# Kernel tuning notes

Measured on AMD Instinct MI355X. Metric: run time of the kernel, lower is better.

Reference implementation:

```python
import jax, jax.numpy as jnp
import numpy as np

GRAVITY, MAIN_THRUST, SIDE_TORQUE, DT = 10.0, 6.0, 1.0, 0.02
H_OBS = jnp.array([[1, 0, 0, 0, 0, 0],
                   [0, 1, 0, 0, 0, 0],
                   [0, 0, 0, 0, 1, 0]], dtype=jnp.float32)  # (3,6)


def build_psd(log_diag, off_diag, dim):
    rows, cols = np.tril_indices(dim, -1)  # row-major, same order as torch.tril_indices
    L = jnp.zeros((dim, dim), dtype=log_diag.dtype)
    L = L.at[jnp.arange(dim), jnp.arange(dim)].set(jnp.exp(log_diag))
    L = L.at[rows, cols].set(off_diag)
    return L @ L.T + 1e-6 * jnp.eye(dim, dtype=log_diag.dtype)


def setup_inputs() -> dict:
    key = jax.random.key(0)
    B = 524288
    ks = jax.random.split(key, 8)
    z = jax.random.normal(ks[0], (B, 3), dtype=jnp.float32)
    u = jax.random.uniform(ks[1], (B, 2), dtype=jnp.float32)
    x_prev = jax.random.normal(ks[2], (B, 6), dtype=jnp.float32)
    A = 0.1 * jax.random.normal(ks[3], (B, 6, 6), dtype=jnp.float32)
    P_prev = jnp.einsum('bij,bkj->bik', A, A) + 0.5 * jnp.eye(6, dtype=jnp.float32)
    q_log_diag = jnp.array([-3.0, -3.0, -2.0, -2.0, -3.0, -2.0], dtype=jnp.float32)
    q_off_diag = 0.01 * jax.random.normal(ks[4], (15,), dtype=jnp.float32)
    r_log_diag = jnp.array([-2.0, -2.0, -2.0], dtype=jnp.float32)
    r_off_diag = 0.01 * jax.random.normal(ks[5], (3,), dtype=jnp.float32)
    return {"z": z, "u": u, "x_prev": x_prev, "P_prev": P_prev,
            "q_log_diag": q_log_diag, "q_off_diag": q_off_diag,
            "r_log_diag": r_log_diag, "r_off_diag": r_off_diag}


def _dynamics(x, u):
    px, py, vx, vy, theta, omega = (x[:, i] for i in range(6))
    main_power = jnp.clip(u[:, 0], 0.0, 1.0)
    lateral = u[:, 1]
    sin_th, cos_th = jnp.sin(theta), jnp.cos(theta)
    ax = -MAIN_THRUST * sin_th * main_power
    ay = MAIN_THRUST * cos_th * main_power - GRAVITY
    alpha = SIDE_TORQUE * lateral
    new_vx = vx + ax * DT
    new_vy = vy + ay * DT
    new_omega = omega + alpha * DT
    new_px = px + new_vx * DT
    new_py = py + new_vy * DT
    new_theta = theta + new_omega * DT
    return jnp.stack([new_px, new_py, new_vx, new_vy, new_theta, new_omega], axis=-1)


def _dynamics_jacobian(x, u):
    B = x.shape[0]
    theta = x[:, 4]
    main_power = jnp.clip(u[:, 0], 0.0, 1.0)
    sin_th, cos_th = jnp.sin(theta), jnp.cos(theta)
    Tm = MAIN_THRUST * main_power
    d = jnp.arange(6)
    F = jnp.zeros((B, 6, 6), dtype=x.dtype).at[:, d, d].set(1.0)
    F = F.at[:, 0, 2].set(DT).at[:, 1, 3].set(DT).at[:, 4, 5].set(DT)
    F = F.at[:, 2, 4].set(-Tm * cos_th * DT)
    F = F.at[:, 3, 4].set(-Tm * sin_th * DT)
    F = F.at[:, 0, 4].set(-Tm * cos_th * (DT * DT))
    F = F.at[:, 1, 4].set(-Tm * sin_th * (DT * DT))
    return F


def reference(z, u, x_prev, P_prev, q_log_diag, q_off_diag, r_log_diag, r_off_diag):
    Q = build_psd(q_log_diag, q_off_diag, 6)
    R = build_psd(r_log_diag, r_off_diag, 3)
    H = H_OBS
    # predict
    x_pred = _dynamics(x_prev, u)                              # (B,6)
    F = _dynamics_jacobian(x_prev, u)                          # (B,6,6)
    P_pred = jnp.einsum('bij,bjk,blk->bil', F, P_prev, F) + Q  # F P F^T + Q
    # update
    z_pred = jnp.einsum('ij,bj->bi', H, x_pred)                # (B,3)
    y = z - z_pred
    HP = jnp.einsum('ij,bjk->bik', H, P_pred)                  # (B,3,6)
    S = jnp.einsum('bij,kj->bik', HP, H) + R                   # (B,3,3)
    K = jnp.swapaxes(jnp.linalg.solve(S, HP), -1, -2)          # (B,6,3)
    x_upd = x_pred + jnp.einsum('bij,bj->bi', K, y)
    IKH = jnp.eye(6, dtype=x_pred.dtype) - jnp.einsum('bij,jk->bik', K, H)
    P_upd = (jnp.einsum('bij,bjk,blk->bil', IKH, P_pred, IKH)
             + jnp.einsum('bij,jk,blk->bil', K, R, K))          # Joseph form
    return (x_upd, P_upd)
```

## Files before the change

### kernel.cpp

```cpp
#include <hip/hip_runtime.h>

namespace {
constexpr float GRAVITY     = 10.0f;
constexpr float MAIN_THRUST = 6.0f;
constexpr float DT          = 0.02f;
constexpr int   BLK         = 128;
constexpr int   ROWPAD      = 44;
}

__global__ void qr_precompute(const float* __restrict__ qld,
                              const float* __restrict__ qod,
                              const float* __restrict__ rld,
                              const float* __restrict__ rod,
                              float* __restrict__ out)
{
    if (threadIdx.x != 0 || blockIdx.x != 0) return;
    float L[6][6];
    for (int i = 0; i < 6; ++i)
        for (int j = 0; j < 6; ++j) L[i][j] = 0.0f;
    for (int i = 0; i < 6; ++i) L[i][i] = expf(qld[i]);
    L[1][0] = qod[0];
    L[2][0] = qod[1];  L[2][1] = qod[2];
    L[3][0] = qod[3];  L[3][1] = qod[4];  L[3][2] = qod[5];
    L[4][0] = qod[6];  L[4][1] = qod[7];  L[4][2] = qod[8];  L[4][3] = qod[9];
    L[5][0] = qod[10]; L[5][1] = qod[11]; L[5][2] = qod[12]; L[5][3] = qod[13];
    L[5][4] = qod[14];
    for (int i = 0; i < 6; ++i)
        for (int j = 0; j < 6; ++j) {
            float s = 0.0f;
            const int m = i < j ? i : j;
            for (int k = 0; k <= m; ++k) s += L[i][k] * L[j][k];
            if (i == j) s += 1e-6f;
            out[i * 6 + j] = s;
        }
    const float rd0 = expf(rld[0]), rd1 = expf(rld[1]), rd2 = expf(rld[2]);
    const float ro0 = rod[0], ro1 = rod[1], ro2 = rod[2];
    out[36] = rd0 * rd0 + 1e-6f;
    out[37] = ro0 * rd0;
    out[38] = ro0 * ro0 + rd1 * rd1 + 1e-6f;
    out[39] = ro1 * rd0;
    out[40] = ro1 * ro0 + ro2 * rd1;
    out[41] = ro1 * ro1 + ro2 * ro2 + rd2 * rd2 + 1e-6f;
}

__global__ __launch_bounds__(BLK) void ekf_kernel(
    const float* __restrict__ z,
    const float* __restrict__ u,
    const float* __restrict__ x_prev,
    const float* __restrict__ P_prev,
    const float* __restrict__ qr,
    float* __restrict__ x_out,
    float* __restrict__ P_out,
    int B)
{
    __shared__ float smem[BLK * ROWPAD];

    const int t = threadIdx.x;
    const long long blockElem0 = (long long)blockIdx.x * BLK;
    const long long elemsLeft  = (long long)B - blockElem0;
    const int nElem  = elemsLeft >= BLK ? BLK : (int)elemsLeft;
    const int count4 = nElem * 9;

    {
        const float4* gP4 = reinterpret_cast<const float4*>(P_prev + blockElem0 * 36);
        #pragma unroll
        for (int k = 0; k < 9; ++k) {
            const int g4 = t + k * BLK;
            if (g4 < count4) {
                const float4 v = gP4[g4];
                const int elem = g4 / 9;
                const int off4 = g4 % 9;
                *reinterpret_cast<float4*>(&smem[elem * ROWPAD + off4 * 4]) = v;
            }
        }
    }
    __syncthreads();

    const bool valid = (t < nElem);
    const long long b = blockElem0 + t;

    if (valid) {
        const float R00 = qr[36], R10 = qr[37], R11 = qr[38];
        const float R20 = qr[39], R21 = qr[40], R22 = qr[41];

        const float2* xp2 = reinterpret_cast<const float2*>(x_prev + 6 * b);
        const float2 x01 = xp2[0], x23 = xp2[1], x45 = xp2[2];
        const float px = x01.x, py = x01.y, vx = x23.x, vy = x23.y;
        const float th = x45.x, om = x45.y;

        const float2 uu = *reinterpret_cast<const float2*>(u + 2 * b);
        const float mp  = fminf(fmaxf(uu.x, 0.0f), 1.0f);
        const float lat = uu.y;

        float s_th, c_th;
        __sincosf(th, &s_th, &c_th);

        const float Tm  = MAIN_THRUST * mp;
        const float ax  = -Tm * s_th;
        const float ay  =  Tm * c_th - GRAVITY;
        const float nvx = vx + ax * DT;
        const float nvy = vy + ay * DT;
        const float nom = om + lat * DT;
        const float npx = px + nvx * DT;
        const float npy = py + nvy * DT;
        const float nth = th + nom * DT;
        const float xp[6] = {npx, npy, nvx, nvy, nth, nom};

        const float f24 = -Tm * c_th * DT;
        const float f34 = -Tm * s_th * DT;
        const float f04 = f24 * DT;
        const float f14 = f34 * DT;

        float P[36];
        const float* myrow = &smem[t * ROWPAD];
        #pragma unroll
        for (int k = 0; k < 9; ++k) {
            const float4 v = *reinterpret_cast<const float4*>(&myrow[k * 4]);
            P[4 * k + 0] = v.x; P[4 * k + 1] = v.y;
            P[4 * k + 2] = v.z; P[4 * k + 3] = v.w;
        }

        #pragma unroll
        for (int j = 0; j < 6; ++j) {
            P[0 * 6 + j] += DT * P[2 * 6 + j] + f04 * P[4 * 6 + j];
            P[1 * 6 + j] += DT * P[3 * 6 + j] + f14 * P[4 * 6 + j];
            P[2 * 6 + j] += f24 * P[4 * 6 + j];
            P[3 * 6 + j] += f34 * P[4 * 6 + j];
            P[4 * 6 + j] += DT * P[5 * 6 + j];
        }
        #pragma unroll
        for (int i = 0; i < 6; ++i) {
            const float m0 = P[i * 6 + 0], m1 = P[i * 6 + 1], m2 = P[i * 6 + 2];
            const float m3 = P[i * 6 + 3], m4 = P[i * 6 + 4], m5 = P[i * 6 + 5];
            P[i * 6 + 0] = m0 + DT * m2 + f04 * m4 + qr[i * 6 + 0];
            P[i * 6 + 1] = m1 + DT * m3 + f14 * m4 + qr[i * 6 + 1];
            P[i * 6 + 2] = m2 + f24 * m4 + qr[i * 6 + 2];
            P[i * 6 + 3] = m3 + f34 * m4 + qr[i * 6 + 3];
            P[i * 6 + 4] = m4 + DT * m5 + qr[i * 6 + 4];
            P[i * 6 + 5] = m5 + qr[i * 6 + 5];
        }

        const float* zp = z + 3 * b;
        const float y0 = zp[0] - npx;
        const float y1 = zp[1] - npy;
        const float y2 = zp[2] - nth;

        const float s00 = P[0 * 6 + 0] + R00;
        const float s01 = P[0 * 6 + 1] + R10;
        const float s02 = P[0 * 6 + 4] + R20;
        const float s10 = P[1 * 6 + 0] + R10;
        const float s11 = P[1 * 6 + 1] + R11;
        const float s12 = P[1 * 6 + 4] + R21;
        const float s20 = P[4 * 6 + 0] + R20;
        const float s21 = P[4 * 6 + 1] + R21;
        const float s22 = P[4 * 6 + 4] + R22;

        const float det = s00 * (s11 * s22 - s12 * s21)
                        + s01 * (s12 * s20 - s10 * s22)
                        + s02 * (s10 * s21 - s11 * s20);
        const float invd = 1.0f / det;
        const float i00 = (s11 * s22 - s12 * s21) * invd;
        const float i01 = (s02 * s21 - s01 * s22) * invd;
        const float i02 = (s01 * s12 - s02 * s11) * invd;
        const float i10 = (s12 * s20 - s10 * s22) * invd;
        const float i11 = (s00 * s22 - s02 * s20) * invd;
        const float i12 = (s02 * s10 - s00 * s12) * invd;
        const float i20 = (s10 * s21 - s11 * s20) * invd;
        const float i21 = (s01 * s20 - s00 * s21) * invd;
        const float i22 = (s00 * s11 - s01 * s10) * invd;

        float r0[6], r1[6], r4[6];
        #pragma unroll
        for (int j = 0; j < 6; ++j) {
            r0[j] = P[0 * 6 + j];
            r1[j] = P[1 * 6 + j];
            r4[j] = P[4 * 6 + j];
        }

        float K[6][3];
        #pragma unroll
        for (int i = 0; i < 6; ++i) {
            const float hp0 = r0[i], hp1 = r1[i], hp2 = r4[i];
            K[i][0] = i00 * hp0 + i01 * hp1 + i02 * hp2;
            K[i][1] = i10 * hp0 + i11 * hp1 + i12 * hp2;
            K[i][2] = i20 * hp0 + i21 * hp1 + i22 * hp2;
        }

        float2* xo2 = reinterpret_cast<float2*>(x_out + 6 * b);
        float xu[6];
        #pragma unroll
        for (int i = 0; i < 6; ++i)
            xu[i] = xp[i] + K[i][0] * y0 + K[i][1] * y1 + K[i][2] * y2;
        xo2[0] = make_float2(xu[0], xu[1]);
        xo2[1] = make_float2(xu[2], xu[3]);
        xo2[2] = make_float2(xu[4], xu[5]);

        #pragma unroll
        for (int i = 0; i < 6; ++i)
            #pragma unroll
            for (int j = 0; j < 6; ++j)
                P[i * 6 + j] -= K[i][0] * r0[j] + K[i][1] * r1[j] + K[i][2] * r4[j];

        float* myrowW = &smem[t * ROWPAD];
        #pragma unroll
        for (int k = 0; k < 9; ++k) {
            float4 v;
            v.x = P[4 * k + 0]; v.y = P[4 * k + 1];
            v.z = P[4 * k + 2]; v.w = P[4 * k + 3];
            *reinterpret_cast<float4*>(&myrowW[k * 4]) = v;
        }
    }
    __syncthreads();

    {
        float4* oP4 = reinterpret_cast<float4*>(P_out + blockElem0 * 36);
        #pragma unroll
        for (int k = 0; k < 9; ++k) {
            const int g4 = t + k * BLK;
            if (g4 < count4) {
                const int elem = g4 / 9;
                const int off4 = g4 % 9;
                oP4[g4] = *reinterpret_cast<const float4*>(&smem[elem * ROWPAD + off4 * 4]);
            }
        }
    }
}

extern "C" void kernel_launch(void* const* d_in, const int* in_sizes, int n_in,
                              void* d_out, int out_size, void* d_ws, size_t ws_size,
                              hipStream_t stream) {
    const float* z          = (const float*)d_in[0];
    const float* u          = (const float*)d_in[1];
    const float* x_prev     = (const float*)d_in[2];
    const float* P_prev     = (const float*)d_in[3];
    const float* q_log_diag = (const float*)d_in[4];
    const float* q_off_diag = (const float*)d_in[5];
    const float* r_log_diag = (const float*)d_in[6];
    const float* r_off_diag = (const float*)d_in[7];

    const int B = in_sizes[0] / 3;
    float* x_out = (float*)d_out;
    float* P_out = (float*)d_out + (size_t)B * 6;
    float* qrbuf = (float*)d_ws;

    qr_precompute<<<1, 64, 0, stream>>>(q_log_diag, q_off_diag,
                                        r_log_diag, r_off_diag, qrbuf);

    const int grid = (B + BLK - 1) / BLK;
    ekf_kernel<<<grid, BLK, 0, stream>>>(z, u, x_prev, P_prev, qrbuf,
                                         x_out, P_out, B);
}
```

Baseline: 186.4 us.

## Process two chunks per block with register prefetch and nontemporal memory ops

Each block now handles two 256-element chunks. The second chunk's P_prev tile is prefetched into registers while the first chunk is staged and computed. Global loads and stores of P and x use nontemporal builtins, and the block size rises to 256 with a launch-bounds occupancy hint. The goal is to hide memory latency in this bandwidth-bound kernel and avoid cache pollution. The cost is higher register pressure from the 36 extra prefetch registers and half as many blocks in the grid.

New measurement: 186.9 us. Within noise of the previous version (+0.2%).

```diff
diff --git a/kernel.cpp b/kernel.cpp
--- a/kernel.cpp
+++ b/kernel.cpp
@@ -4,9 +4,13 @@
 constexpr float GRAVITY     = 10.0f;
 constexpr float MAIN_THRUST = 6.0f;
 constexpr float DT          = 0.02f;
-constexpr int   BLK         = 128;
+constexpr int   BLK         = 256;
+constexpr int   CHUNK       = 256;
 constexpr int   ROWPAD      = 44;
 }
+
+typedef float nfloat4 __attribute__((ext_vector_type(4)));
+typedef float nfloat2 __attribute__((ext_vector_type(2)));
 
 __global__ void qr_precompute(const float* __restrict__ qld,
                               const float* __restrict__ qod,
@@ -43,7 +47,43 @@
     out[41] = ro1 * ro1 + ro2 * ro2 + rd2 * rd2 + 1e-6f;
 }
 
-__global__ __launch_bounds__(BLK) void ekf_kernel(
+__device__ __forceinline__ void load_chunk(const nfloat4* __restrict__ gP4,
+                                           int t, int count4, nfloat4 pf[9]) {
+    #pragma unroll
+    for (int k = 0; k < 9; ++k) {
+        const int g4 = t + k * BLK;
+        if (g4 < count4) pf[k] = __builtin_nontemporal_load(&gP4[g4]);
+    }
+}
+
+__device__ __forceinline__ void stage_in(const nfloat4 pf[9], float* smem,
+                                         int t, int count4) {
+    #pragma unroll
+    for (int k = 0; k < 9; ++k) {
+        const int g4 = t + k * BLK;
+        if (g4 < count4) {
+            const int elem = g4 / 9;
+            const int off4 = g4 % 9;
+            *reinterpret_cast<nfloat4*>(&smem[elem * ROWPAD + off4 * 4]) = pf[k];
+        }
+    }
+}
+
+__device__ __forceinline__ void stage_out(nfloat4* __restrict__ oP4,
+                                          const float* smem, int t, int count4) {
+    #pragma unroll
+    for (int k = 0; k < 9; ++k) {
+        const int g4 = t + k * BLK;
+        if (g4 < count4) {
+            const int elem = g4 / 9;
+            const int off4 = g4 % 9;
+            const nfloat4 v = *reinterpret_cast<const nfloat4*>(&smem[elem * ROWPAD + off4 * 4]);
+            __builtin_nontemporal_store(v, &oP4[g4]);
+        }
+    }
+}
+
+__global__ __launch_bounds__(BLK, 3) void ekf_kernel(
     const float* __restrict__ z,
     const float* __restrict__ u,
     const float* __restrict__ x_prev,
@@ -55,40 +95,32 @@
 {
     __shared__ float smem[BLK * ROWPAD];
 
-    const int t = threadIdx.x;
-    const long long blockElem0 = (long long)blockIdx.x * BLK;
-    const long long elemsLeft  = (long long)B - blockElem0;
-    const int nElem  = elemsLeft >= BLK ? BLK : (int)elemsLeft;
-    const int count4 = nElem * 9;
-
-    {
-        const float4* gP4 = reinterpret_cast<const float4*>(P_prev + blockElem0 * 36);
-        #pragma unroll
-        for (int k = 0; k < 9; ++k) {
-            const int g4 = t + k * BLK;
-            if (g4 < count4) {
-                const float4 v = gP4[g4];
-                const int elem = g4 / 9;
-                const int off4 = g4 % 9;
-                *reinterpret_cast<float4*>(&smem[elem * ROWPAD + off4 * 4]) = v;
-            }
-        }
-    }
-    __syncthreads();
-
-    const bool valid = (t < nElem);
-    const long long b = blockElem0 + t;
-
-    if (valid) {
+    const int t  = threadIdx.x;
+    const int c0 = blockIdx.x;
+    const int c1 = blockIdx.x + gridDim.x;
+    const int nchunk = (B + CHUNK - 1) / CHUNK;
+
+    const int base0   = c0 * CHUNK;
+    const int nE0     = min(B - base0, CHUNK);
+    const int count40 = nE0 * 9;
+    const bool has1   = (c1 < nchunk);
+    const int base1   = has1 ? c1 * CHUNK : 0;
+    const int nE1     = has1 ? min(B - base1, CHUNK) : 0;
+    const int count41 = nE1 * 9;
+
+    auto do_compute = [&](int base, int nE) {
+        if (t >= nE) return;
+        const int b = base + t;
+
         const float R00 = qr[36], R10 = qr[37], R11 = qr[38];
         const float R20 = qr[39], R21 = qr[40], R22 = qr[41];
 
-        const float2* xp2 = reinterpret_cast<const float2*>(x_prev + 6 * b);
-        const float2 x01 = xp2[0], x23 = xp2[1], x45 = xp2[2];
+        const nfloat2* xp2 = reinterpret_cast<const nfloat2*>(x_prev + 6 * b);
+        const nfloat2 x01 = xp2[0], x23 = xp2[1], x45 = xp2[2];
         const float px = x01.x, py = x01.y, vx = x23.x, vy = x23.y;
         const float th = x45.x, om = x45.y;
 
-        const float2 uu = *reinterpret_cast<const float2*>(u + 2 * b);
+        const nfloat2 uu = *reinterpret_cast<const nfloat2*>(u + 2 * b);
         const float mp  = fminf(fmaxf(uu.x, 0.0f), 1.0f);
         const float lat = uu.y;
 
@@ -115,7 +147,7 @@
         const float* myrow = &smem[t * ROWPAD];
         #pragma unroll
         for (int k = 0; k < 9; ++k) {
-            const float4 v = *reinterpret_cast<const float4*>(&myrow[k * 4]);
+            const nfloat4 v = *reinterpret_cast<const nfloat4*>(&myrow[k * 4]);
             P[4 * k + 0] = v.x; P[4 * k + 1] = v.y;
             P[4 * k + 2] = v.z; P[4 * k + 3] = v.w;
         }
@@ -186,14 +218,17 @@
             K[i][2] = i20 * hp0 + i21 * hp1 + i22 * hp2;
         }
 
-        float2* xo2 = reinterpret_cast<float2*>(x_out + 6 * b);
+        nfloat2* xo2 = reinterpret_cast<nfloat2*>(x_out + 6 * b);
         float xu[6];
         #pragma unroll
         for (int i = 0; i < 6; ++i)
             xu[i] = xp[i] + K[i][0] * y0 + K[i][1] * y1 + K[i][2] * y2;
-        xo2[0] = make_float2(xu[0], xu[1]);
-        xo2[1] = make_float2(xu[2], xu[3]);
-        xo2[2] = make_float2(xu[4], xu[5]);
+        nfloat2 o01; o01.x = xu[0]; o01.y = xu[1];
+        nfloat2 o23; o23.x = xu[2]; o23.y = xu[3];
+        nfloat2 o45; o45.x = xu[4]; o45.y = xu[5];
+        __builtin_nontemporal_store(o01, &xo2[0]);
+        __builtin_nontemporal_store(o23, &xo2[1]);
+        __builtin_nontemporal_store(o45, &xo2[2]);
 
         #pragma unroll
         for (int i = 0; i < 6; ++i)
@@ -204,25 +239,36 @@
         float* myrowW = &smem[t * ROWPAD];
         #pragma unroll
         for (int k = 0; k < 9; ++k) {
-            float4 v;
+            nfloat4 v;
             v.x = P[4 * k + 0]; v.y = P[4 * k + 1];
             v.z = P[4 * k + 2]; v.w = P[4 * k + 3];
-            *reinterpret_cast<float4*>(&myrowW[k * 4]) = v;
-        }
-    }
+            *reinterpret_cast<nfloat4*>(&myrowW[k * 4]) = v;
+        }
+    };
+
+    nfloat4 pfA[9];
+    load_chunk(reinterpret_cast<const nfloat4*>(P_prev + (size_t)base0 * 36),
+               t, count40, pfA);
+
+    stage_in(pfA, smem, t, count40);
+    nfloat4 pfB[9];
+    if (has1)
+        load_chunk(reinterpret_cast<const nfloat4*>(P_prev + (size_t)base1 * 36),
+                   t, count41, pfB);
     __syncthreads();
-
-    {
-        float4* oP4 = reinterpret_cast<float4*>(P_out + blockElem0 * 36);
-        #pragma unroll
-        for (int k = 0; k < 9; ++k) {
-            const int g4 = t + k * BLK;
-            if (g4 < count4) {
-                const int elem = g4 / 9;
-                const int off4 = g4 % 9;
-                oP4[g4] = *reinterpret_cast<const float4*>(&smem[elem * ROWPAD + off4 * 4]);
-            }
-        }
+    do_compute(base0, nE0);
+    __syncthreads();
+    stage_out(reinterpret_cast<nfloat4*>(P_out + (size_t)base0 * 36),
+              smem, t, count40);
+
+    if (has1) {
+        __syncthreads();
+        stage_in(pfB, smem, t, count41);
+        __syncthreads();
+        do_compute(base1, nE1);
+        __syncthreads();
+        stage_out(reinterpret_cast<nfloat4*>(P_out + (size_t)base1 * 36),
+                  smem, t, count41);
     }
 }
 
@@ -246,7 +292,8 @@
     qr_precompute<<<1, 64, 0, stream>>>(q_log_diag, q_off_diag,
                                         r_log_diag, r_off_diag, qrbuf);
 
-    const int grid = (B + BLK - 1) / BLK;
+    const int nchunk = (B + CHUNK - 1) / CHUNK;
+    const int grid   = (nchunk + 1) / 2;
     ekf_kernel<<<grid, BLK, 0, stream>>>(z, u, x_prev, P_prev, qrbuf,
                                          x_out, P_out, B);
 }
```
